# Kernel tuning notes

Measured on AMD Instinct MI355X. Metric: run time of the kernel, lower is better.

The kernel has to match this reference:

```python
import jax, jax.numpy as jnp
import numpy as np

B, S, E = 2, 2048, 2048
H, KV, HD = 16, 4, 128          # attn heads, kv heads, head_dim = E//H
GROUPS = H // KV
I = 8192                        # intermediate_size
EPS = 1e-6
ROPE_THETA = 10000.0
SCALE = HD ** -0.5


def _rope_tables(seq_len, head_dim, dtype=jnp.float32):
    inv_freq = 1.0 / (ROPE_THETA ** (jnp.arange(0, head_dim, 2, dtype=jnp.float32) / head_dim))
    pos = jnp.arange(seq_len, dtype=jnp.float32)
    ang = pos[:, None] * inv_freq[None, :]            # [S, HD/2]
    emb = jnp.concatenate([ang, ang], axis=-1)        # [S, HD]
    return jnp.cos(emb).astype(dtype), jnp.sin(emb).astype(dtype)


def _rotate_half(x):
    x1, x2 = jnp.split(x, 2, axis=-1)
    return jnp.concatenate([-x2, x1], axis=-1)


def _apply_rope(x, cos, sin):
    # x: [B, h, S, HD]; cos/sin: [S, HD]
    return x * cos[None, None] + _rotate_half(x) * sin[None, None]


def _rmsnorm(x, w, eps=EPS):
    var = jnp.mean(jnp.square(x), axis=-1, keepdims=True)
    return x * jax.lax.rsqrt(var + eps) * w


def setup_inputs() -> dict:
    key = jax.random.key(0)
    ks = jax.random.split(key, 12)
    sd = lambda fan_in: 1.0 / np.sqrt(fan_in)
    inp = {
        "x": jax.random.normal(ks[0], (B, S, E), dtype=jnp.float32),
        "attn_mask": jnp.zeros((B, 1, S, S), dtype=jnp.bool_),
        "wq": jax.random.normal(ks[1], (E, E), dtype=jnp.float32) * sd(E),
        "bq": jnp.zeros((E,), dtype=jnp.float32),
        "wkv": jax.random.normal(ks[2], (2 * KV * HD, E), dtype=jnp.float32) * sd(E),
        "bkv": jnp.zeros((2 * KV * HD,), dtype=jnp.float32),
        "wo": jax.random.normal(ks[3], (E, E), dtype=jnp.float32) * sd(E),
        "w_gate": jax.random.normal(ks[4], (I, E), dtype=jnp.float32) * sd(E),
        "w_up": jax.random.normal(ks[5], (I, E), dtype=jnp.float32) * sd(E),
        "w_down": jax.random.normal(ks[6], (E, I), dtype=jnp.float32) * sd(I),
        "norm1_w": jnp.ones((E,), dtype=jnp.float32),
        "norm2_w": jnp.ones((E,), dtype=jnp.float32),
    }
    return inp


def reference(x, attn_mask, wq, bq, wkv, bkv, wo, w_gate, w_up, w_down, norm1_w, norm2_w):
    # ---- attention block ----
    y = _rmsnorm(x, norm1_w)
    q = y @ wq.T + bq                                     # [B,S,E]
    kv = y @ wkv.T + bkv                                  # [B,S,2*KV*HD]
    k, v = jnp.split(kv, 2, axis=-1)
    q = q.reshape(B, S, H, HD).transpose(0, 2, 1, 3)      # [B,H,S,HD]
    k = k.reshape(B, S, KV, HD).transpose(0, 2, 1, 3)     # [B,KV,S,HD]
    v = v.reshape(B, S, KV, HD).transpose(0, 2, 1, 3)
    cos, sin = _rope_tables(S, HD, dtype=q.dtype)
    q = _apply_rope(q, cos, sin)
    k = _apply_rope(k, cos, sin)
    # GQA expand kv heads
    k = jnp.repeat(k, GROUPS, axis=1)                     # [B,H,S,HD]
    v = jnp.repeat(v, GROUPS, axis=1)
    # NOTE: source Qwen2Attention.forward never applies attn_mask — faithful here.
    scores = jnp.einsum('bhsd,bhtd->bhst', q, k) * SCALE  # [B,H,S,S]
    attn = jax.nn.softmax(scores, axis=-1)
    o = jnp.einsum('bhst,bhtd->bhsd', attn, v)            # [B,H,S,HD]
    o = o.transpose(0, 2, 1, 3).reshape(B, S, E) @ wo.T
    x = x + o
    # ---- MLP block (SwiGLU) ----
    y = _rmsnorm(x, norm2_w)
    h = jax.nn.silu(y @ w_gate.T) * (y @ w_up.T)          # [B,S,I]
    x = x + h @ w_down.T
    return x
```

## Files before the change

kernel.cpp:

```cpp
#include <hip/hip_runtime.h>

typedef __bf16 bf16;
typedef __bf16 bf16x8 __attribute__((ext_vector_type(8)));
typedef __bf16 bf16x4 __attribute__((ext_vector_type(4)));
typedef float f32x4 __attribute__((ext_vector_type(4)));

#define DEV __device__ __forceinline__

constexpr int B_ = 2, S_ = 2048, E_ = 2048, H_ = 16, KVH_ = 4, HD_ = 128, I_ = 8192;
constexpr int KVROW = 2 * KVH_ * HD_;
constexpr float EPS_ = 1e-6f;
constexpr float SCALE_ = 0.08838834764831845f;

DEV void gload_lds16(const bf16* g, bf16* l) {
  __builtin_amdgcn_global_load_lds(
      (const __attribute__((address_space(1))) void*)g,
      (__attribute__((address_space(3))) void*)l, 16, 0, 0);
}

__global__ __launch_bounds__(256) void cvt6_k(const float* __restrict__ s0, const float* __restrict__ s1,
                                              const float* __restrict__ s2, const float* __restrict__ s3,
                                              const float* __restrict__ s4, const float* __restrict__ s5,
                                              bf16* __restrict__ dst) {
  constexpr size_t N0 = 4194304, N1 = 2097152, N2 = 4194304,
                   N3 = 16777216, N4 = 16777216, N5 = 16777216;
  constexpr size_t TOT = N0 + N1 + N2 + N3 + N4 + N5;
  for (size_t i = ((size_t)blockIdx.x * 256 + threadIdx.x) * 8; i < TOT;
       i += (size_t)gridDim.x * 256 * 8) {
    size_t off = i; const float* sp;
    if (off < N0) sp = s0;
    else if ((off -= N0) < N1) sp = s1;
    else if ((off -= N1) < N2) sp = s2;
    else if ((off -= N2) < N3) sp = s3;
    else if ((off -= N3) < N4) sp = s4;
    else { off -= N4; sp = s5; }
    const float4* p = (const float4*)(sp + off);
    float4 a = p[0], b = p[1];
    bf16x8 o;
    o[0]=(bf16)a.x; o[1]=(bf16)a.y; o[2]=(bf16)a.z; o[3]=(bf16)a.w;
    o[4]=(bf16)b.x; o[5]=(bf16)b.y; o[6]=(bf16)b.z; o[7]=(bf16)b.w;
    *(bf16x8*)(dst + i) = o;
  }
}

template <typename InT>
__global__ __launch_bounds__(256) void rmsnorm_k(const InT* __restrict__ x,
                                                 const float* __restrict__ w,
                                                 bf16* __restrict__ y) {
  const int row = blockIdx.x, t = threadIdx.x;
  const size_t base = (size_t)row * E_ + t * 8;
  float v[8];
  if constexpr (sizeof(InT) == 2) {
    bf16x8 d = *(const bf16x8*)(x + base);
#pragma unroll
    for (int j = 0; j < 8; ++j) v[j] = (float)d[j];
  } else {
    const float4* p = (const float4*)(x + base);
    float4 a = p[0], b2 = p[1];
    v[0]=a.x; v[1]=a.y; v[2]=a.z; v[3]=a.w; v[4]=b2.x; v[5]=b2.y; v[6]=b2.z; v[7]=b2.w;
  }
  float ss = 0.f;
#pragma unroll
  for (int j = 0; j < 8; ++j) ss += v[j] * v[j];
#pragma unroll
  for (int off = 32; off; off >>= 1) ss += __shfl_xor(ss, off);
  __shared__ float red[4];
  if ((t & 63) == 0) red[t >> 6] = ss;
  __syncthreads();
  ss = red[0] + red[1] + red[2] + red[3];
  const float sc = rsqrtf(ss * (1.0f / E_) + EPS_);
  const float4* wp = (const float4*)(w + t * 8);
  float4 wa = wp[0], wb = wp[1];
  float wv[8] = {wa.x, wa.y, wa.z, wa.w, wb.x, wb.y, wb.z, wb.w};
  bf16x8 o;
#pragma unroll
  for (int j = 0; j < 8; ++j) o[j] = (bf16)(v[j] * sc * wv[j]);
  *(bf16x8*)(y + base) = o;
}

__global__ __launch_bounds__(256) void rope_k(bf16* __restrict__ q, bf16* __restrict__ kvb) {
  const int gid = blockIdx.x * 256 + threadIdx.x;
  const int d = gid & 63;
  const int r = gid >> 6;
  const int hh = r % (H_ + KVH_);
  const int s = (r / (H_ + KVH_)) % S_;
  const int b = r / ((H_ + KVH_) * S_);
  bf16* p = (hh < H_) ? (q + (size_t)(b * S_ + s) * E_ + hh * HD_)
                      : (kvb + (size_t)(b * S_ + s) * KVROW + (hh - H_) * HD_);
  const float invf = exp2f(-(float)d * (13.287712379549449f / 64.f));
  float sn, cs;
  sincosf((float)s * invf, &sn, &cs);
  const float x1 = (float)p[d], x2 = (float)p[d + 64];
  p[d] = (bf16)(x1 * cs - x2 * sn);
  p[d + 64] = (bf16)(x2 * cs + x1 * sn);
}

DEV void stage_half(const bf16* Gb, int Kst, bf16* dst, int t, int kbase, int h) {
#pragma unroll
  for (int i = 0; i < 2; ++i) {
    const int c = t + i * 512;
    const int row = c >> 3, slot = c & 7;
    gload_lds16(Gb + (size_t)(h * 128 + row) * Kst + kbase + ((slot ^ (row & 7)) << 3),
                dst + h * 8192 + c * 8);
  }
}

template <int EPI>
__global__ __launch_bounds__(512, 2) void gemm8p(const bf16* __restrict__ A,
                                                 const bf16* __restrict__ W,
                                                 const void* __restrict__ ext,
                                                 void* __restrict__ out,
                                                 int M, int N, int K) {
  __shared__ bf16 As[2][16384];
  __shared__ bf16 Bs[2][16384];
  const int t = threadIdx.x, lane = t & 63, w = t >> 6;
  const int g = lane >> 4, l15 = lane & 15;
  const int wm = w >> 2, wn = w & 3;
  const int nbm = M >> 8, nwg = nbm * (N >> 8);
  int lin = blockIdx.x;
  { const int qq = nwg >> 3, rr = nwg & 7, xcd = lin & 7, idx = lin >> 3;
    lin = (xcd < rr ? xcd * (qq + 1) : rr * (qq + 1) + (xcd - rr) * qq) + idx; }
  const int bm = lin % nbm, bn = lin / nbm;

  const bf16* Ab = A + (size_t)bm * 256 * K;
  const bf16* Wb = W + (size_t)bn * 256 * K;
  const int T = K >> 6;

  f32x4 acc[8][4];
#pragma unroll
  for (int i = 0; i < 8; ++i)
#pragma unroll
    for (int j = 0; j < 4; ++j) acc[i][j] = {0.f, 0.f, 0.f, 0.f};

  stage_half(Wb, K, Bs[0], t, 0, 0);
  stage_half(Wb, K, Bs[0], t, 0, 1);
  stage_half(Ab, K, As[0], t, 0, 1);
  stage_half(Ab, K, As[0], t, 0, 0);
  if (T > 1) {
    stage_half(Wb, K, Bs[1], t, 64, 0);
    stage_half(Wb, K, Bs[1], t, 64, 1);
  }
  asm volatile("s_waitcnt vmcnt(4)" ::: "memory");
  __builtin_amdgcn_s_barrier();
  __builtin_amdgcn_sched_barrier(0);

  int p = 0;
  const int arb = wm * 128, brb = wn * 64;
  for (int tau = 0; tau < T; ++tau, p ^= 1) {
    bf16* Ap = As[p]; bf16* Bp = Bs[p]; bf16* An = As[p ^ 1];
    const int kb1 = (tau + 1) << 6, kb2 = (tau + 2) << 6;
    bf16x8 bfr[4][2];
#pragma unroll
    for (int q = 0; q < 4; ++q) {
      bf16x8 afr[2][2];
#pragma unroll
      for (int j = 0; j < 2; ++j) {
        const int ar = arb + q * 32 + j * 16 + l15;
#pragma unroll
        for (int ks = 0; ks < 2; ++ks)
          afr[j][ks] = *(const bf16x8*)&Ap[ar * 64 + ((((ks << 2) + g) ^ (ar & 7)) << 3)];
      }
      if (q == 0) {
#pragma unroll
        for (int nt = 0; nt < 4; ++nt) {
          const int br = brb + nt * 16 + l15;
#pragma unroll
          for (int ks = 0; ks < 2; ++ks)
            bfr[nt][ks] = *(const bf16x8*)&Bp[br * 64 + ((((ks << 2) + g) ^ (br & 7)) << 3)];
        }
        if (kb1 < K) stage_half(Ab, K, An, t, kb1, 1);
      } else if (q == 1) {
        if (kb1 < K) stage_half(Ab, K, An, t, kb1, 0);
      } else if (q == 2) {
        if (kb2 < K) stage_half(Wb, K, Bp, t, kb2, 0);
      } else {
        if (kb2 < K) {
          stage_half(Wb, K, Bp, t, kb2, 1);
          asm volatile("s_waitcnt vmcnt(4)" ::: "memory");
        } else {
          asm volatile("s_waitcnt vmcnt(0)" ::: "memory");
        }
      }
      __builtin_amdgcn_s_barrier();
      __builtin_amdgcn_sched_barrier(0);
      __builtin_amdgcn_s_setprio(1);
#pragma unroll
      for (int ks = 0; ks < 2; ++ks)
#pragma unroll
        for (int j = 0; j < 2; ++j)
#pragma unroll
          for (int nt = 0; nt < 4; ++nt)
            acc[q * 2 + j][nt] = __builtin_amdgcn_mfma_f32_16x16x32_bf16(
                afr[j][ks], bfr[nt][ks], acc[q * 2 + j][nt], 0, 0, 0);
      __builtin_amdgcn_s_setprio(0);
      __builtin_amdgcn_sched_barrier(0);
      __builtin_amdgcn_s_barrier();
    }
  }

  const size_t row0 = (size_t)bm * 256 + wm * 128;
  const int col0 = bn * 256 + wn * 64;
#pragma unroll
  for (int fr = 0; fr < 8; ++fr)
#pragma unroll
    for (int nt = 0; nt < 4; ++nt) {
      const int col = col0 + nt * 16 + l15;
#pragma unroll
      for (int r = 0; r < 4; ++r) {
        const size_t idx = (row0 + fr * 16 + g * 4 + r) * N + col;
        float v = acc[fr][nt][r];
        if constexpr (EPI == 2) {
          const float gv = (float)((const bf16*)ext)[idx];
          v *= gv / (1.f + __expf(-gv));
        }
        ((bf16*)out)[idx] = (bf16)v;
      }
    }
}

template <int EPI, bool WB>
__global__ __launch_bounds__(256, 2) void gemm_bt(const bf16* __restrict__ A,
                                                  const void* __restrict__ Wp,
                                                  const float* __restrict__ bias,
                                                  const void* __restrict__ ext,
                                                  void* __restrict__ out,
                                                  int M, int N, int K) {
  constexpr int BK = 64;
  __shared__ bf16 As[128 * BK];
  __shared__ bf16 Bs[128 * BK];
  const int t = threadIdx.x, lane = t & 63, w = t >> 6;
  const int g = lane >> 4, l15 = lane & 15;
  const int bm = blockIdx.y, bn = blockIdx.x;
  const int wm = w >> 1, wn = w & 1;
  f32x4 acc[4][4];
#pragma unroll
  for (int i = 0; i < 4; ++i)
#pragma unroll
    for (int j = 0; j < 4; ++j) acc[i][j] = {0.f, 0.f, 0.f, 0.f};

  const bf16* Ab = A + (size_t)bm * 128 * K;

  for (int k0 = 0; k0 < K; k0 += BK) {
    __syncthreads();
#pragma unroll
    for (int i = 0; i < 4; ++i) {
      const int c = t + i * 256;
      const int row = c >> 3, slot = c & 7;
      gload_lds16(Ab + (size_t)row * K + k0 + ((slot ^ (row & 7)) << 3), &As[c * 8]);
    }
    if constexpr (WB) {
      const bf16* Wb = (const bf16*)Wp + (size_t)bn * 128 * K;
#pragma unroll
      for (int i = 0; i < 4; ++i) {
        const int c = t + i * 256;
        const int row = c >> 3, slot = c & 7;
        gload_lds16(Wb + (size_t)row * K + k0 + ((slot ^ (row & 7)) << 3), &Bs[c * 8]);
      }
    } else {
      const float* Wb = (const float*)Wp + (size_t)bn * 128 * K;
#pragma unroll
      for (int i = 0; i < 4; ++i) {
        const int c = t + i * 256;
        const int row = c >> 3, slot = c & 7;
        const float4* wp = (const float4*)(Wb + (size_t)row * K + k0 + slot * 8);
        float4 w0 = wp[0], w1 = wp[1];
        bf16x8 pk;
        pk[0] = (bf16)w0.x; pk[1] = (bf16)w0.y; pk[2] = (bf16)w0.z; pk[3] = (bf16)w0.w;
        pk[4] = (bf16)w1.x; pk[5] = (bf16)w1.y; pk[6] = (bf16)w1.z; pk[7] = (bf16)w1.w;
        *(bf16x8*)&Bs[row * BK + ((slot ^ (row & 7)) << 3)] = pk;
      }
    }
    __syncthreads();
#pragma unroll
    for (int ks = 0; ks < 2; ++ks) {
      bf16x8 af[4], bfv[4];
#pragma unroll
      for (int mt = 0; mt < 4; ++mt) {
        const int row = wm * 64 + mt * 16 + l15;
        af[mt] = *(const bf16x8*)&As[row * BK + (((ks * 4 + g) ^ (row & 7)) << 3)];
      }
#pragma unroll
      for (int nt = 0; nt < 4; ++nt) {
        const int row = wn * 64 + nt * 16 + l15;
        bfv[nt] = *(const bf16x8*)&Bs[row * BK + (((ks * 4 + g) ^ (row & 7)) << 3)];
      }
#pragma unroll
      for (int mt = 0; mt < 4; ++mt)
#pragma unroll
        for (int nt = 0; nt < 4; ++nt)
          acc[mt][nt] = __builtin_amdgcn_mfma_f32_16x16x32_bf16(af[mt], bfv[nt], acc[mt][nt], 0, 0, 0);
    }
  }

  const int row0 = bm * 128 + wm * 64;
  const int col0 = bn * 128 + wn * 64;
#pragma unroll
  for (int nt = 0; nt < 4; ++nt) {
    const int col = col0 + nt * 16 + l15;
    const float bv = bias ? bias[col] : 0.f;
#pragma unroll
    for (int mt = 0; mt < 4; ++mt) {
#pragma unroll
      for (int r = 0; r < 4; ++r) {
        const int rowi = row0 + mt * 16 + g * 4 + r;
        const size_t idx = (size_t)rowi * N + col;
        float v = acc[mt][nt][r] + bv;
        if constexpr (EPI == 0) {
          ((bf16*)out)[idx] = (bf16)v;
        } else if constexpr (EPI == 1) {
          v += ((const float*)ext)[idx];
          ((bf16*)out)[idx] = (bf16)v;
        } else if constexpr (EPI == 2) {
          const float gv = (float)((const bf16*)ext)[idx];
          const float sg = gv / (1.f + __expf(-gv));
          ((bf16*)out)[idx] = (bf16)(sg * v);
        } else {
          v += (float)((const bf16*)ext)[idx];
          ((float*)out)[idx] = v;
        }
      }
    }
  }
}

__global__ __launch_bounds__(256, 2) void attn_k(const bf16* __restrict__ qb,
                                                 const bf16* __restrict__ kvb,
                                                 bf16* __restrict__ ob) {
  __shared__ bf16 Ks[64 * 128];
  __shared__ bf16 Vt[128 * 64];
  __shared__ bf16 Ps[4][32 * 64];
  const int t = threadIdx.x, lane = t & 63, w = t >> 6;
  const int g = lane >> 4, l15 = lane & 15;
  const int b = blockIdx.z, h = blockIdx.y;
  const int kvh = h >> 2;
  const int q0 = blockIdx.x * 128 + w * 32;

  bf16x8 qf[2][4];
#pragma unroll
  for (int qt = 0; qt < 2; ++qt)
#pragma unroll
    for (int ks = 0; ks < 4; ++ks)
      qf[qt][ks] = *(const bf16x8*)(qb + (size_t)(b * S_ + q0 + qt * 16 + l15) * E_ + h * HD_ + ks * 32 + g * 8);

  f32x4 o[8][2];
#pragma unroll
  for (int i = 0; i < 8; ++i) { o[i][0] = {0.f,0.f,0.f,0.f}; o[i][1] = {0.f,0.f,0.f,0.f}; }
  float mA[2] = {-1e30f, -1e30f}, lA[2] = {0.f, 0.f};

  for (int s0 = 0; s0 < S_; s0 += 64) {
    __syncthreads();
#pragma unroll
    for (int i = 0; i < 4; ++i) {
      const int c = t + i * 256;
      const int row = c >> 4, slot = c & 15;
      gload_lds16(kvb + (size_t)(b * S_ + s0 + row) * KVROW + kvh * HD_ + ((slot ^ (row & 15)) << 3),
                  &Ks[c * 8]);
    }
#pragma unroll
    for (int i = 0; i < 4; ++i) {
      const int c = t + i * 256;
      const int d = c & 127, kvc = c >> 7;
      const bf16* vs = kvb + (size_t)(b * S_ + s0 + kvc * 8) * KVROW + KVH_ * HD_ + kvh * HD_ + d;
      bf16x8 pk;
#pragma unroll
      for (int j = 0; j < 8; ++j) pk[j] = vs[(size_t)j * KVROW];
      *(bf16x8*)&Vt[d * 64 + ((kvc ^ (d & 7)) << 3)] = pk;
    }
    __syncthreads();

    f32x4 sc[2][4];
#pragma unroll
    for (int qt = 0; qt < 2; ++qt)
#pragma unroll
      for (int c = 0; c < 4; ++c) sc[qt][c] = {0.f,0.f,0.f,0.f};
#pragma unroll
    for (int ks = 0; ks < 4; ++ks) {
      bf16x8 kf[4];
#pragma unroll
      for (int c = 0; c < 4; ++c) {
        const int kv = c * 16 + l15;
        kf[c] = *(const bf16x8*)&Ks[kv * 128 + (((ks * 4 + g) ^ (kv & 15)) << 3)];
      }
#pragma unroll
      for (int c = 0; c < 4; ++c) {
        sc[0][c] = __builtin_amdgcn_mfma_f32_16x16x32_bf16(kf[c], qf[0][ks], sc[0][c], 0, 0, 0);
        sc[1][c] = __builtin_amdgcn_mfma_f32_16x16x32_bf16(kf[c], qf[1][ks], sc[1][c], 0, 0, 0);
      }
    }

    float corr[2];
#pragma unroll
    for (int qt = 0; qt < 2; ++qt) {
      float tm = sc[qt][0][0];
#pragma unroll
      for (int c = 0; c < 4; ++c)
#pragma unroll
        for (int r = 0; r < 4; ++r) tm = fmaxf(tm, sc[qt][c][r]);
      tm = fmaxf(tm, __shfl_xor(tm, 16));
      tm = fmaxf(tm, __shfl_xor(tm, 32));
      const float mn = fmaxf(mA[qt], tm);
      corr[qt] = __expf((mA[qt] - mn) * SCALE_);
      mA[qt] = mn;
      float ps = 0.f;
      const int q = qt * 16 + l15;
#pragma unroll
      for (int c = 0; c < 4; ++c)
#pragma unroll
        for (int r = 0; r < 4; ++r) {
          const float p = __expf((sc[qt][c][r] - mn) * SCALE_);
          ps += p;
          const int kv = c * 16 + g * 4 + r;
          Ps[w][q * 64 + (((kv >> 3) ^ (q & 7)) << 3) + (kv & 7)] = (bf16)p;
        }
      ps += __shfl_xor(ps, 16);
      ps += __shfl_xor(ps, 32);
      lA[qt] = lA[qt] * corr[qt] + ps;
#pragma unroll
      for (int dt = 0; dt < 8; ++dt) o[dt][qt] *= corr[qt];
    }
    asm volatile("s_waitcnt lgkmcnt(0)" ::: "memory");
#pragma unroll
    for (int ks = 0; ks < 2; ++ks) {
      bf16x8 pf[2];
#pragma unroll
      for (int qt = 0; qt < 2; ++qt) {
        const int q = qt * 16 + l15;
        pf[qt] = *(const bf16x8*)&Ps[w][q * 64 + (((ks * 4 + g) ^ (q & 7)) << 3)];
      }
#pragma unroll
      for (int dt = 0; dt < 8; ++dt) {
        const int d = dt * 16 + l15;
        const bf16x8 vf = *(const bf16x8*)&Vt[d * 64 + (((ks * 4 + g) ^ (d & 7)) << 3)];
        o[dt][0] = __builtin_amdgcn_mfma_f32_16x16x32_bf16(vf, pf[0], o[dt][0], 0, 0, 0);
        o[dt][1] = __builtin_amdgcn_mfma_f32_16x16x32_bf16(vf, pf[1], o[dt][1], 0, 0, 0);
      }
    }
  }

  const float inv0 = 1.f / lA[0], inv1 = 1.f / lA[1];
  __syncthreads();
  bf16* bb = (w < 2) ? &Ks[(w & 1) * 4096] : &Vt[(w & 1) * 4096];
#pragma unroll
  for (int dt = 0; dt < 8; ++dt)
#pragma unroll
    for (int qt = 0; qt < 2; ++qt) {
      const float iv = qt ? inv1 : inv0;
      bf16x4 pk;
#pragma unroll
      for (int r = 0; r < 4; ++r) pk[r] = (bf16)(o[dt][qt][r] * iv);
      const int q = qt * 16 + l15;
      const int s16 = (dt * 2 + (g >> 1)) ^ (q & 15);
      *(bf16x4*)&bb[q * 128 + (s16 << 3) + ((g & 1) << 2)] = pk;
    }
  asm volatile("s_waitcnt lgkmcnt(0)" ::: "memory");
#pragma unroll
  for (int it = 0; it < 8; ++it) {
    const int c = lane + it * 64;
    const int q = c >> 4, s16 = c & 15;
    const bf16x8 vv = *(const bf16x8*)&bb[q * 128 + ((s16 ^ (q & 15)) << 3)];
    *(bf16x8*)(ob + (size_t)(b * S_ + q0 + q) * E_ + h * HD_ + s16 * 8) = vv;
  }
}

extern "C" void kernel_launch(void* const* d_in, const int* in_sizes, int n_in,
                              void* d_out, int out_size, void* d_ws, size_t ws_size,
                              hipStream_t stream) {
  const float* x   = (const float*)d_in[0];
  const float* wq  = (const float*)d_in[2];
  const float* bq  = (const float*)d_in[3];
  const float* wkv = (const float*)d_in[4];
  const float* bkv = (const float*)d_in[5];
  const float* wo  = (const float*)d_in[6];
  const float* wg  = (const float*)d_in[7];
  const float* wu  = (const float*)d_in[8];
  const float* wd  = (const float*)d_in[9];
  const float* n1  = (const float*)d_in[10];
  const float* n2  = (const float*)d_in[11];
  float* out = (float*)d_out;
  char* ws = (char*)d_ws;
  bf16* y  = (bf16*)(ws);
  bf16* q  = (bf16*)(ws + (16ull << 20));
  bf16* kv = (bf16*)(ws + (32ull << 20));
  bf16* x1 = (bf16*)(ws + (40ull << 20));
  bf16* gh = (bf16*)(ws + (56ull << 20));
  bf16* o  = y;
  bf16* y2 = y;
  bf16* wqb  = (bf16*)(ws + (120ull << 20));
  bf16* wkvb = (bf16*)(ws + (128ull << 20));
  bf16* wob  = (bf16*)(ws + (132ull << 20));
  bf16* wgb  = (bf16*)(ws + (140ull << 20));
  bf16* wub  = (bf16*)(ws + (172ull << 20));
  bf16* wdb  = (bf16*)(ws + (204ull << 20));
  const int M = B_ * S_;
  const bool tierA = ws_size >= (236ull << 20);

  if (tierA)
    cvt6_k<<<2048, 256, 0, stream>>>(wq, wkv, wo, wg, wu, wd, wqb);

  rmsnorm_k<float><<<M, 256, 0, stream>>>(x, n1, y);
  if (tierA) {
    gemm_bt<0, true><<<dim3(E_ / 128, M / 128), 256, 0, stream>>>(y, wqb, bq, nullptr, q, M, E_, E_);
    gemm_bt<0, true><<<dim3(KVROW / 128, M / 128), 256, 0, stream>>>(y, wkvb, bkv, nullptr, kv, M, KVROW, E_);
  } else {
    gemm_bt<0, false><<<dim3(E_ / 128, M / 128), 256, 0, stream>>>(y, wq, bq, nullptr, q, M, E_, E_);
    gemm_bt<0, false><<<dim3(KVROW / 128, M / 128), 256, 0, stream>>>(y, wkv, bkv, nullptr, kv, M, KVROW, E_);
  }
  rope_k<<<(B_ * S_ * (H_ + KVH_) * 64) / 256, 256, 0, stream>>>(q, kv);
  attn_k<<<dim3(S_ / 128, H_, B_), 256, 0, stream>>>(q, kv, o);
  if (tierA) {
    gemm_bt<1, true><<<dim3(E_ / 128, M / 128), 256, 0, stream>>>(o, wob, nullptr, x, x1, M, E_, E_);
    rmsnorm_k<bf16><<<M, 256, 0, stream>>>(x1, n2, y2);
    gemm8p<0><<<(I_ / 256) * (M / 256), 512, 0, stream>>>(y2, wgb, nullptr, gh, M, I_, E_);
    gemm8p<2><<<(I_ / 256) * (M / 256), 512, 0, stream>>>(y2, wub, gh, gh, M, I_, E_);
    gemm_bt<3, true><<<dim3(E_ / 128, M / 128), 256, 0, stream>>>(gh, wdb, nullptr, x1, out, M, E_, I_);
  } else {
    gemm_bt<1, false><<<dim3(E_ / 128, M / 128), 256, 0, stream>>>(o, wo, nullptr, x, x1, M, E_, E_);
    rmsnorm_k<bf16><<<M, 256, 0, stream>>>(x1, n2, y2);
    gemm_bt<0, false><<<dim3(I_ / 128, M / 128), 256, 0, stream>>>(y2, wg, nullptr, nullptr, gh, M, I_, E_);
    gemm_bt<2, false><<<dim3(I_ / 128, M / 128), 256, 0, stream>>>(y2, wu, nullptr, gh, gh, M, I_, E_);
    gemm_bt<3, false><<<dim3(E_ / 128, M / 128), 256, 0, stream>>>(gh, wd, nullptr, x1, out, M, E_, I_);
  }
}
```

Baseline: 821.1 us.

## Restructure GEMM main loop into two halves with fewer barriers per K-step

```diff
diff --git a/kernel.cpp b/kernel.cpp
--- a/kernel.cpp
+++ b/kernel.cpp
@@ -132,57 +132,83 @@
 #pragma unroll
     for (int j = 0; j < 4; ++j) acc[i][j] = {0.f, 0.f, 0.f, 0.f};
 
+  stage_half(Ab, K, As[0], t, 0, 0);
+  stage_half(Ab, K, As[0], t, 0, 1);
   stage_half(Wb, K, Bs[0], t, 0, 0);
   stage_half(Wb, K, Bs[0], t, 0, 1);
-  stage_half(Ab, K, As[0], t, 0, 1);
-  stage_half(Ab, K, As[0], t, 0, 0);
   if (T > 1) {
     stage_half(Wb, K, Bs[1], t, 64, 0);
     stage_half(Wb, K, Bs[1], t, 64, 1);
-  }
-  asm volatile("s_waitcnt vmcnt(4)" ::: "memory");
+    asm volatile("s_waitcnt vmcnt(4)" ::: "memory");
+  } else {
+    asm volatile("s_waitcnt vmcnt(0)" ::: "memory");
+  }
   __builtin_amdgcn_s_barrier();
   __builtin_amdgcn_sched_barrier(0);
 
   int p = 0;
   const int arb = wm * 128, brb = wn * 64;
   for (int tau = 0; tau < T; ++tau, p ^= 1) {
-    bf16* Ap = As[p]; bf16* Bp = Bs[p]; bf16* An = As[p ^ 1];
-    const int kb1 = (tau + 1) << 6, kb2 = (tau + 2) << 6;
+    bf16* Ap = As[p]; bf16* Bp = Bs[p];
+    if (tau + 1 < T) {
+      stage_half(Ab, K, As[p ^ 1], t, (tau + 1) << 6, 0);
+      stage_half(Ab, K, As[p ^ 1], t, (tau + 1) << 6, 1);
+    }
     bf16x8 bfr[4][2];
 #pragma unroll
-    for (int q = 0; q < 4; ++q) {
-      bf16x8 afr[2][2];
+    for (int nt = 0; nt < 4; ++nt) {
+      const int br = brb + nt * 16 + l15;
+#pragma unroll
+      for (int ks = 0; ks < 2; ++ks)
+        bfr[nt][ks] = *(const bf16x8*)&Bp[br * 64 + ((((ks << 2) + g) ^ (br & 7)) << 3)];
+    }
+    {
+      bf16x8 af0[2][2], af1[2][2];
 #pragma unroll
       for (int j = 0; j < 2; ++j) {
-        const int ar = arb + q * 32 + j * 16 + l15;
-#pragma unroll
-        for (int ks = 0; ks < 2; ++ks)
-          afr[j][ks] = *(const bf16x8*)&Ap[ar * 64 + ((((ks << 2) + g) ^ (ar & 7)) << 3)];
-      }
-      if (q == 0) {
-#pragma unroll
-        for (int nt = 0; nt < 4; ++nt) {
-          const int br = brb + nt * 16 + l15;
-#pragma unroll
-          for (int ks = 0; ks < 2; ++ks)
-            bfr[nt][ks] = *(const bf16x8*)&Bp[br * 64 + ((((ks << 2) + g) ^ (br & 7)) << 3)];
+        const int a0 = arb + j * 16 + l15, a1 = arb + 32 + j * 16 + l15;
+#pragma unroll
+        for (int ks = 0; ks < 2; ++ks) {
+          af0[j][ks] = *(const bf16x8*)&Ap[a0 * 64 + ((((ks << 2) + g) ^ (a0 & 7)) << 3)];
+          af1[j][ks] = *(const bf16x8*)&Ap[a1 * 64 + ((((ks << 2) + g) ^ (a1 & 7)) << 3)];
         }
-        if (kb1 < K) stage_half(Ab, K, An, t, kb1, 1);
-      } else if (q == 1) {
-        if (kb1 < K) stage_half(Ab, K, An, t, kb1, 0);
-      } else if (q == 2) {
-        if (kb2 < K) stage_half(Wb, K, Bp, t, kb2, 0);
-      } else {
-        if (kb2 < K) {
-          stage_half(Wb, K, Bp, t, kb2, 1);
-          asm volatile("s_waitcnt vmcnt(4)" ::: "memory");
-        } else {
-          asm volatile("s_waitcnt vmcnt(0)" ::: "memory");
+      }
+      __builtin_amdgcn_s_setprio(1);
+#pragma unroll
+      for (int ks = 0; ks < 2; ++ks)
+#pragma unroll
+        for (int j = 0; j < 2; ++j)
+#pragma unroll
+          for (int nt = 0; nt < 4; ++nt)
+            acc[j][nt] = __builtin_amdgcn_mfma_f32_16x16x32_bf16(
+                af0[j][ks], bfr[nt][ks], acc[j][nt], 0, 0, 0);
+#pragma unroll
+      for (int ks = 0; ks < 2; ++ks)
+#pragma unroll
+        for (int j = 0; j < 2; ++j)
+#pragma unroll
+          for (int nt = 0; nt < 4; ++nt)
+            acc[2 + j][nt] = __builtin_amdgcn_mfma_f32_16x16x32_bf16(
+                af1[j][ks], bfr[nt][ks], acc[2 + j][nt], 0, 0, 0);
+      __builtin_amdgcn_s_setprio(0);
+    }
+    __builtin_amdgcn_s_barrier();
+    __builtin_amdgcn_sched_barrier(0);
+    if (tau + 2 < T) {
+      stage_half(Wb, K, Bp, t, (tau + 2) << 6, 0);
+      stage_half(Wb, K, Bp, t, (tau + 2) << 6, 1);
+    }
+    {
+      bf16x8 af2[2][2], af3[2][2];
+#pragma unroll
+      for (int j = 0; j < 2; ++j) {
+        const int a2 = arb + 64 + j * 16 + l15, a3 = arb + 96 + j * 16 + l15;
+#pragma unroll
+        for (int ks = 0; ks < 2; ++ks) {
+          af2[j][ks] = *(const bf16x8*)&Ap[a2 * 64 + ((((ks << 2) + g) ^ (a2 & 7)) << 3)];
+          af3[j][ks] = *(const bf16x8*)&Ap[a3 * 64 + ((((ks << 2) + g) ^ (a3 & 7)) << 3)];
         }
       }
-      __builtin_amdgcn_s_barrier();
-      __builtin_amdgcn_sched_barrier(0);
       __builtin_amdgcn_s_setprio(1);
 #pragma unroll
       for (int ks = 0; ks < 2; ++ks)
@@ -190,12 +216,22 @@
         for (int j = 0; j < 2; ++j)
 #pragma unroll
           for (int nt = 0; nt < 4; ++nt)
-            acc[q * 2 + j][nt] = __builtin_amdgcn_mfma_f32_16x16x32_bf16(
-                afr[j][ks], bfr[nt][ks], acc[q * 2 + j][nt], 0, 0, 0);
+            acc[4 + j][nt] = __builtin_amdgcn_mfma_f32_16x16x32_bf16(
+                af2[j][ks], bfr[nt][ks], acc[4 + j][nt], 0, 0, 0);
+#pragma unroll
+      for (int ks = 0; ks < 2; ++ks)
+#pragma unroll
+        for (int j = 0; j < 2; ++j)
+#pragma unroll
+          for (int nt = 0; nt < 4; ++nt)
+            acc[6 + j][nt] = __builtin_amdgcn_mfma_f32_16x16x32_bf16(
+                af3[j][ks], bfr[nt][ks], acc[6 + j][nt], 0, 0, 0);
       __builtin_amdgcn_s_setprio(0);
-      __builtin_amdgcn_sched_barrier(0);
-      __builtin_amdgcn_s_barrier();
-    }
+    }
+    if (tau + 2 < T)      asm volatile("s_waitcnt vmcnt(4)" ::: "memory");
+    else if (tau + 1 < T) asm volatile("s_waitcnt vmcnt(0)" ::: "memory");
+    __builtin_amdgcn_s_barrier();
+    __builtin_amdgcn_sched_barrier(0);
   }
 
   const size_t row0 = (size_t)bm * 256 + wm * 128;
```

Result: no change. 813.7 us (-0.9%).
